# Performance work log

Hardware: AMD Instinct MI355X
Metric: run time of the kernel (lower is better)

Reference implementation:

```python
import jax, jax.numpy as jnp
import numpy as np

B, N, H, W = 128, 16384, 512, 512  # frames, points/frame, image height/width


def setup_inputs() -> dict:
    key = jax.random.key(0)
    k1, k2 = jax.random.split(key)
    pts = jax.random.uniform(k1, (B, N, 3), dtype=jnp.float32)
    # columns: x in [0, W-1], y in [0, H-1], intensity in [0, 1]
    outputs = jnp.concatenate(
        [pts[..., 0:1] * (W - 1), pts[..., 1:2] * (H - 1), pts[..., 2:3]], axis=-1
    )
    targets = jax.random.uniform(k2, (B, H, W), dtype=jnp.float32)
    return {"outputs": outputs, "targets": targets}


def _rasterize(outputs, h, w):
    """Bilinear splat of (x, y, intensity) points into a [B, h, w] image."""
    b, n, _ = outputs.shape
    x = jnp.clip(outputs[..., 0], 0.0, w - 1)
    y = jnp.clip(outputs[..., 1], 0.0, h - 1)
    inten = outputs[..., 2]
    x0f = jnp.floor(x)
    y0f = jnp.floor(y)
    fx = x - x0f  # fractional offsets -> bilinear weights
    fy = y - y0f
    x0 = x0f.astype(jnp.int32)
    y0 = y0f.astype(jnp.int32)
    x1 = jnp.minimum(x0 + 1, w - 1)
    y1 = jnp.minimum(y0 + 1, h - 1)
    bidx = jnp.broadcast_to(jnp.arange(b, dtype=jnp.int32)[:, None], (b, n))
    img = jnp.zeros((b, h, w), dtype=outputs.dtype)
    img = img.at[bidx, y0, x0].add(inten * (1 - fx) * (1 - fy))
    img = img.at[bidx, y0, x1].add(inten * fx * (1 - fy))
    img = img.at[bidx, y1, x0].add(inten * (1 - fx) * fy)
    img = img.at[bidx, y1, x1].add(inten * fx * fy)
    return img


def reference(outputs, targets):
    h, w = targets.shape[1], targets.shape[2]
    output_image = _rasterize(outputs, h, w)
    return jnp.mean((output_image - targets) ** 2)
```

## Files before the change

### kernel.cpp

```cpp
#include <hip/hip_runtime.h>

constexpr int B = 128;
constexpr int N = 16384;
constexpr int H = 512;
constexpr int W = 512;
constexpr int HW = H * W;
constexpr long long TOT = (long long)B * HW;

constexpr int TROWS = 16;
constexpr int NTILES = H / TROWS;
constexpr int NBUCKETS = B * NTILES;
constexpr int CAP = 1024;
constexpr int NGROUPS = B * N / 4;
constexpr int BIN_BLOCKS = NGROUPS / 512;
constexpr int TPITCH = 520;
constexpr int TILE_WORDS = TROWS * TPITCH;

__device__ __forceinline__ void lds_add(float* p, float v) {
    __hip_atomic_fetch_add(p, v, __ATOMIC_RELAXED, __HIP_MEMORY_SCOPE_WORKGROUP);
}

__device__ __forceinline__ void pin(float4& v) {
    asm volatile("" : "+v"(v.x), "+v"(v.y), "+v"(v.z), "+v"(v.w));
}

__global__ void __launch_bounds__(512) k_zero(unsigned int* __restrict__ cnt) {
    cnt[blockIdx.x * 512 + threadIdx.x] = 0u;
}

__global__ void __launch_bounds__(512) k_bin(const float4* __restrict__ pts,
                                             float4* __restrict__ buckets,
                                             unsigned int* __restrict__ cnt) {
    __shared__ unsigned int lcnt[NTILES];
    __shared__ unsigned int lbase[NTILES];

    int tid = blockIdx.x * 512 + threadIdx.x;
    int frame = tid >> 12;
    int fb = frame * NTILES;

    if (threadIdx.x < NTILES) lcnt[threadIdx.x] = 0;
    __syncthreads();

    float4 a = pts[tid * 3 + 0];
    float4 b = pts[tid * 3 + 1];
    float4 c = pts[tid * 3 + 2];

    float xs[4] = {a.x, a.w, b.z, c.y};
    float ys[4] = {a.y, b.x, b.w, c.z};
    float is[4] = {a.z, b.y, c.x, c.w};

    int tb0[4], sl0[4], tb1[4], sl1[4];
#pragma unroll
    for (int k = 0; k < 4; ++k) {
        float x = fminf(fmaxf(xs[k], 0.0f), (float)(W - 1));
        float y = fminf(fmaxf(ys[k], 0.0f), (float)(H - 1));
        xs[k] = x; ys[k] = y;
        int y0 = (int)floorf(y);
        int y1 = min(y0 + 1, H - 1);
        int t0 = y0 >> 4;
        int t1 = y1 >> 4;
        tb0[k] = t0;
        sl0[k] = (int)atomicAdd(&lcnt[t0], 1u);
        if (t1 != t0) {
            tb1[k] = t1;
            sl1[k] = (int)atomicAdd(&lcnt[t1], 1u);
        } else {
            tb1[k] = -1; sl1[k] = 0;
        }
    }
    __syncthreads();

    if (threadIdx.x < NTILES)
        lbase[threadIdx.x] = atomicAdd(&cnt[fb + threadIdx.x], lcnt[threadIdx.x]);
    __syncthreads();

#pragma unroll
    for (int k = 0; k < 4; ++k) {
        float4 rec = make_float4(xs[k], ys[k], is[k], 0.0f);
        unsigned s0 = lbase[tb0[k]] + (unsigned)sl0[k];
        if (s0 < (unsigned)CAP)
            buckets[(size_t)(fb + tb0[k]) * CAP + s0] = rec;
        if (tb1[k] >= 0) {
            unsigned s1 = lbase[tb1[k]] + (unsigned)sl1[k];
            if (s1 < (unsigned)CAP)
                buckets[(size_t)(fb + tb1[k]) * CAP + s1] = rec;
        }
    }
}

__device__ __forceinline__ void splat(float4 p, float* __restrict__ tile, int r0) {
    float x = p.x, y = p.y, inten = p.z;
    float x0f = floorf(x), y0f = floorf(y);
    float fx = x - x0f, fy = y - y0f;
    int x0 = (int)x0f, y0 = (int)y0f;
    int x1 = min(x0 + 1, W - 1);
    int y1 = min(y0 + 1, H - 1);
    int ra = y0 - r0;
    int rb = y1 - r0;
    float w00 = inten * (1.0f - fx) * (1.0f - fy);
    float w01 = inten * fx * (1.0f - fy);
    float w10 = inten * (1.0f - fx) * fy;
    float w11 = inten * fx * fy;
    if ((unsigned)ra < (unsigned)TROWS) {
        lds_add(&tile[ra * TPITCH + x0], w00);
        lds_add(&tile[ra * TPITCH + x1], w01);
    }
    if ((unsigned)rb < (unsigned)TROWS) {
        lds_add(&tile[rb * TPITCH + x0], w10);
        lds_add(&tile[rb * TPITCH + x1], w11);
    }
}

__global__ void __launch_bounds__(512) k_tile(const float4* __restrict__ buckets,
                                              const unsigned int* __restrict__ cnt,
                                              const float* __restrict__ tgt,
                                              double* __restrict__ ptile) {
    __shared__ __align__(16) float tile[TILE_WORDS];
    __shared__ double sacc[8];
    int bid = blockIdx.x;
    int frame = bid >> 5;
    int t = bid & (NTILES - 1);
    int r0 = t * TROWS;
    int tid = threadIdx.x;

    const float4* bp = buckets + (size_t)bid * CAP;
    float4 p0 = bp[tid];
    float4 p1 = bp[tid + 512];
    const float4* tg = (const float4*)(tgt + (size_t)frame * HW + (size_t)r0 * W);
    float4 tv0 = tg[tid];
    float4 tv1 = tg[tid + 512];
    float4 tv2 = tg[tid + 1024];
    float4 tv3 = tg[tid + 1536];
    int n = (int)min(cnt[bid], (unsigned)CAP);
    pin(p0); pin(p1); pin(tv0); pin(tv1); pin(tv2); pin(tv3);

    float4* t4 = (float4*)tile;
    float4 z = make_float4(0.f, 0.f, 0.f, 0.f);
    for (int i = tid; i < TILE_WORDS / 4; i += 512)
        t4[i] = z;
    __syncthreads();

    if (tid < n)       splat(p0, tile, r0);
    if (tid + 512 < n) splat(p1, tile, r0);
    __syncthreads();

    float facc = 0.0f;
#pragma unroll
    for (int k = 0; k < 4; ++k) {
        int g = tid + k * 512;
        int r = g >> 7;
        int c = (g & 127) << 2;
        float4 sv = *(const float4*)&tile[r * TPITCH + c];
        float4 tv = (k == 0) ? tv0 : (k == 1) ? tv1 : (k == 2) ? tv2 : tv3;
        float d0 = sv.x - tv.x, d1 = sv.y - tv.y;
        float d2 = sv.z - tv.z, d3 = sv.w - tv.w;
        facc += d0 * d0 + d1 * d1 + d2 * d2 + d3 * d3;
    }

    double acc = (double)facc;
    for (int off = 32; off > 0; off >>= 1)
        acc += __shfl_down(acc, off, 64);
    int lane = tid & 63;
    int wave = tid >> 6;
    if (lane == 0) sacc[wave] = acc;
    __syncthreads();
    if (tid == 0) {
        double s = 0.0;
#pragma unroll
        for (int wv = 0; wv < 8; ++wv) s += sacc[wv];
        ptile[bid] = s;
    }
}

__global__ void __launch_bounds__(512) k_final(const double* __restrict__ ptile,
                                               float* __restrict__ out) {
    double acc = 0.0;
    for (int i = threadIdx.x; i < NBUCKETS; i += 512)
        acc += ptile[i];
    for (int off = 32; off > 0; off >>= 1)
        acc += __shfl_down(acc, off, 64);
    __shared__ double sacc[8];
    int lane = threadIdx.x & 63;
    int wave = threadIdx.x >> 6;
    if (lane == 0) sacc[wave] = acc;
    __syncthreads();
    if (threadIdx.x == 0) {
        double s = 0.0;
#pragma unroll
        for (int wv = 0; wv < 8; ++wv) s += sacc[wv];
        out[0] = (float)(s / (double)TOT);
    }
}

extern "C" void kernel_launch(void* const* d_in, const int* in_sizes, int n_in,
                              void* d_out, int out_size, void* d_ws, size_t ws_size,
                              hipStream_t stream) {
    const float* pts = (const float*)d_in[0];
    const float* tgt = (const float*)d_in[1];
    float* out = (float*)d_out;

    unsigned int* cnt = (unsigned int*)d_ws;
    double* ptile = (double*)((char*)d_ws + 16384);
    float4* buckets = (float4*)((char*)d_ws + 65536);

    k_zero<<<NBUCKETS / 512, 512, 0, stream>>>(cnt);
    k_bin<<<BIN_BLOCKS, 512, 0, stream>>>((const float4*)pts, buckets, cnt);
    k_tile<<<NBUCKETS, 512, 0, stream>>>(buckets, cnt, tgt, ptile);
    k_final<<<1, 512, 0, stream>>>(ptile, out);
}
```

Baseline: 80.81 us.

## Process four tiles per block with double-buffered prefetch of next tile's data

k_tile now handles four consecutive row tiles per workgroup instead of one, launching a quarter as many blocks. While the current tile is zeroed and splatted, it issues the next tile's bucket points, target rows and count into a second register buffer. Barriers now wait only on LDS counters, so those global loads stay in flight across barriers. The per-wave reduction also moves from double to float shuffles before the double conversion; this costs more registers and slightly changes summation precision.

```diff
diff --git a/kernel.cpp b/kernel.cpp
--- a/kernel.cpp
+++ b/kernel.cpp
@@ -15,13 +15,16 @@
 constexpr int BIN_BLOCKS = NGROUPS / 512;
 constexpr int TPITCH = 520;
 constexpr int TILE_WORDS = TROWS * TPITCH;
+constexpr int TPB = 4;
+constexpr int TILE_BLOCKS = NBUCKETS / TPB;
 
 __device__ __forceinline__ void lds_add(float* p, float v) {
     __hip_atomic_fetch_add(p, v, __ATOMIC_RELAXED, __HIP_MEMORY_SCOPE_WORKGROUP);
 }
 
-__device__ __forceinline__ void pin(float4& v) {
-    asm volatile("" : "+v"(v.x), "+v"(v.y), "+v"(v.z), "+v"(v.w));
+__device__ __forceinline__ void BAR() {
+    asm volatile("s_waitcnt lgkmcnt(0)" ::: "memory");
+    __builtin_amdgcn_s_barrier();
 }
 
 __global__ void __launch_bounds__(512) k_zero(unsigned int* __restrict__ cnt) {
@@ -117,59 +120,77 @@
                                               double* __restrict__ ptile) {
     __shared__ __align__(16) float tile[TILE_WORDS];
     __shared__ double sacc[8];
-    int bid = blockIdx.x;
-    int frame = bid >> 5;
-    int t = bid & (NTILES - 1);
-    int r0 = t * TROWS;
     int tid = threadIdx.x;
-
-    const float4* bp = buckets + (size_t)bid * CAP;
-    float4 p0 = bp[tid];
-    float4 p1 = bp[tid + 512];
-    const float4* tg = (const float4*)(tgt + (size_t)frame * HW + (size_t)r0 * W);
-    float4 tv0 = tg[tid];
-    float4 tv1 = tg[tid + 512];
-    float4 tv2 = tg[tid + 1024];
-    float4 tv3 = tg[tid + 1536];
-    int n = (int)min(cnt[bid], (unsigned)CAP);
-    pin(p0); pin(p1); pin(tv0); pin(tv1); pin(tv2); pin(tv3);
+    int base = blockIdx.x * TPB;
+
+    float4 P[2][2];
+    float4 TV[2][4];
+    int    NN[2];
+
+#define LOADT(slot, tj) do {                                                   \
+        int tid_ = base + (tj);                                                \
+        const float4* bp_ = buckets + (size_t)tid_ * CAP;                      \
+        P[slot][0] = bp_[tid];                                                 \
+        P[slot][1] = bp_[tid + 512];                                           \
+        const float4* tg_ = (const float4*)(tgt + (size_t)(tid_ >> 5) * HW +   \
+                                            (size_t)(tid_ & 31) * TROWS * W);  \
+        TV[slot][0] = tg_[tid];                                                \
+        TV[slot][1] = tg_[tid + 512];                                          \
+        TV[slot][2] = tg_[tid + 1024];                                         \
+        TV[slot][3] = tg_[tid + 1536];                                         \
+        NN[slot] = (int)min(cnt[tid_], (unsigned)CAP);                         \
+    } while (0)
+
+    LOADT(0, 0);
 
     float4* t4 = (float4*)tile;
-    float4 z = make_float4(0.f, 0.f, 0.f, 0.f);
-    for (int i = tid; i < TILE_WORDS / 4; i += 512)
-        t4[i] = z;
-    __syncthreads();
-
-    if (tid < n)       splat(p0, tile, r0);
-    if (tid + 512 < n) splat(p1, tile, r0);
-    __syncthreads();
-
-    float facc = 0.0f;
-#pragma unroll
-    for (int k = 0; k < 4; ++k) {
-        int g = tid + k * 512;
-        int r = g >> 7;
-        int c = (g & 127) << 2;
-        float4 sv = *(const float4*)&tile[r * TPITCH + c];
-        float4 tv = (k == 0) ? tv0 : (k == 1) ? tv1 : (k == 2) ? tv2 : tv3;
-        float d0 = sv.x - tv.x, d1 = sv.y - tv.y;
-        float d2 = sv.z - tv.z, d3 = sv.w - tv.w;
-        facc += d0 * d0 + d1 * d1 + d2 * d2 + d3 * d3;
-    }
-
-    double acc = (double)facc;
-    for (int off = 32; off > 0; off >>= 1)
-        acc += __shfl_down(acc, off, 64);
-    int lane = tid & 63;
-    int wave = tid >> 6;
-    if (lane == 0) sacc[wave] = acc;
-    __syncthreads();
-    if (tid == 0) {
-        double s = 0.0;
-#pragma unroll
-        for (int wv = 0; wv < 8; ++wv) s += sacc[wv];
-        ptile[bid] = s;
-    }
+#pragma unroll
+    for (int j = 0; j < TPB; ++j) {
+        const int cur = j & 1, nxt = cur ^ 1;
+        int tile_id = base + j;
+        int r0 = (tile_id & (NTILES - 1)) * TROWS;
+
+        float4 z = make_float4(0.f, 0.f, 0.f, 0.f);
+        for (int i = tid; i < TILE_WORDS / 4; i += 512)
+            t4[i] = z;
+
+        if (j + 1 < TPB) LOADT(nxt, j + 1);
+
+        BAR();
+
+        int n = NN[cur];
+        if (tid < n)       splat(P[cur][0], tile, r0);
+        if (tid + 512 < n) splat(P[cur][1], tile, r0);
+
+        BAR();
+
+        float facc = 0.0f;
+#pragma unroll
+        for (int k = 0; k < 4; ++k) {
+            int g = tid + k * 512;
+            int r = g >> 7;
+            int c = (g & 127) << 2;
+            float4 sv = *(const float4*)&tile[r * TPITCH + c];
+            float4 tv = TV[cur][k];
+            float d0 = sv.x - tv.x, d1 = sv.y - tv.y;
+            float d2 = sv.z - tv.z, d3 = sv.w - tv.w;
+            facc += d0 * d0 + d1 * d1 + d2 * d2 + d3 * d3;
+        }
+
+        for (int off = 32; off > 0; off >>= 1)
+            facc += __shfl_down(facc, off, 64);
+        int lane = tid & 63;
+        int wave = tid >> 6;
+        if (lane == 0) sacc[wave] = (double)facc;
+        BAR();
+        if (tid == 0) {
+            double s = 0.0;
+#pragma unroll
+            for (int wv = 0; wv < 8; ++wv) s += sacc[wv];
+            ptile[tile_id] = s;
+        }
+    }
+#undef LOADT
 }
 
 __global__ void __launch_bounds__(512) k_final(const double* __restrict__ ptile,
@@ -205,6 +226,6 @@
 
     k_zero<<<NBUCKETS / 512, 512, 0, stream>>>(cnt);
     k_bin<<<BIN_BLOCKS, 512, 0, stream>>>((const float4*)pts, buckets, cnt);
-    k_tile<<<NBUCKETS, 512, 0, stream>>>(buckets, cnt, tgt, ptile);
+    k_tile<<<TILE_BLOCKS, 512, 0, stream>>>(buckets, cnt, tgt, ptile);
     k_final<<<1, 512, 0, stream>>>(ptile, out);
 }
```

Result: slower. 83.88 us (+3.8%).

## Split tile splat and MSE into separate kernels with fp16 intermediate image

Applied to the files above, without the earlier changes.

Halves the row tile and bucket capacity, then breaks the fused splat+MSE kernel in two. The splat kernel writes the rasterized tile to global memory as packed fp16, and a separate grid-stride kernel reads that image alongside the targets to compute the squared error. The intent is to take the target loads out of the LDS-atomic splat kernel and stream them in a simple bandwidth-bound pass. In exchange it adds an extra global round trip of the image (fp16, 32 MB write plus read), which loses precision in the rasterized values and adds a kernel launch.

```diff
diff --git a/kernel.cpp b/kernel.cpp
--- a/kernel.cpp
+++ b/kernel.cpp
@@ -1,4 +1,5 @@
 #include <hip/hip_runtime.h>
+#include <hip/hip_fp16.h>
 
 constexpr int B = 128;
 constexpr int N = 16384;
@@ -7,21 +8,28 @@
 constexpr int HW = H * W;
 constexpr long long TOT = (long long)B * HW;
 
-constexpr int TROWS = 16;
+constexpr int TROWS = 8;
 constexpr int NTILES = H / TROWS;
 constexpr int NBUCKETS = B * NTILES;
-constexpr int CAP = 1024;
+constexpr int CAP = 512;
 constexpr int NGROUPS = B * N / 4;
 constexpr int BIN_BLOCKS = NGROUPS / 512;
 constexpr int TPITCH = 520;
 constexpr int TILE_WORDS = TROWS * TPITCH;
+constexpr int MSE_BLOCKS = 2048;
 
 __device__ __forceinline__ void lds_add(float* p, float v) {
     __hip_atomic_fetch_add(p, v, __ATOMIC_RELAXED, __HIP_MEMORY_SCOPE_WORKGROUP);
 }
 
-__device__ __forceinline__ void pin(float4& v) {
-    asm volatile("" : "+v"(v.x), "+v"(v.y), "+v"(v.z), "+v"(v.w));
+__device__ __forceinline__ unsigned pack2(float a, float b) {
+    __half2 h = __floats2half2_rn(a, b);
+    return *reinterpret_cast<unsigned*>(&h);
+}
+
+__device__ __forceinline__ float2 unpack2(unsigned u) {
+    __half2 h = *reinterpret_cast<__half2*>(&u);
+    return __half22float2(h);
 }
 
 __global__ void __launch_bounds__(512) k_zero(unsigned int* __restrict__ cnt) {
@@ -57,8 +65,8 @@
         xs[k] = x; ys[k] = y;
         int y0 = (int)floorf(y);
         int y1 = min(y0 + 1, H - 1);
-        int t0 = y0 >> 4;
-        int t1 = y1 >> 4;
+        int t0 = y0 >> 3;
+        int t1 = y1 >> 3;
         tb0[k] = t0;
         sl0[k] = (int)atomicAdd(&lcnt[t0], 1u);
         if (t1 != t0) {
@@ -88,95 +96,105 @@
     }
 }
 
-__device__ __forceinline__ void splat(float4 p, float* __restrict__ tile, int r0) {
-    float x = p.x, y = p.y, inten = p.z;
-    float x0f = floorf(x), y0f = floorf(y);
-    float fx = x - x0f, fy = y - y0f;
-    int x0 = (int)x0f, y0 = (int)y0f;
-    int x1 = min(x0 + 1, W - 1);
-    int y1 = min(y0 + 1, H - 1);
-    int ra = y0 - r0;
-    int rb = y1 - r0;
-    float w00 = inten * (1.0f - fx) * (1.0f - fy);
-    float w01 = inten * fx * (1.0f - fy);
-    float w10 = inten * (1.0f - fx) * fy;
-    float w11 = inten * fx * fy;
-    if ((unsigned)ra < (unsigned)TROWS) {
-        lds_add(&tile[ra * TPITCH + x0], w00);
-        lds_add(&tile[ra * TPITCH + x1], w01);
-    }
-    if ((unsigned)rb < (unsigned)TROWS) {
-        lds_add(&tile[rb * TPITCH + x0], w10);
-        lds_add(&tile[rb * TPITCH + x1], w11);
-    }
-}
-
-__global__ void __launch_bounds__(512) k_tile(const float4* __restrict__ buckets,
-                                              const unsigned int* __restrict__ cnt,
-                                              const float* __restrict__ tgt,
-                                              double* __restrict__ ptile) {
+__global__ void __launch_bounds__(256) k_splat(const float4* __restrict__ buckets,
+                                               const unsigned int* __restrict__ cnt,
+                                               unsigned* __restrict__ img_u) {
     __shared__ __align__(16) float tile[TILE_WORDS];
-    __shared__ double sacc[8];
     int bid = blockIdx.x;
-    int frame = bid >> 5;
+    int frame = bid >> 6;
     int t = bid & (NTILES - 1);
     int r0 = t * TROWS;
     int tid = threadIdx.x;
 
-    const float4* bp = buckets + (size_t)bid * CAP;
-    float4 p0 = bp[tid];
-    float4 p1 = bp[tid + 512];
-    const float4* tg = (const float4*)(tgt + (size_t)frame * HW + (size_t)r0 * W);
-    float4 tv0 = tg[tid];
-    float4 tv1 = tg[tid + 512];
-    float4 tv2 = tg[tid + 1024];
-    float4 tv3 = tg[tid + 1536];
-    int n = (int)min(cnt[bid], (unsigned)CAP);
-    pin(p0); pin(p1); pin(tv0); pin(tv1); pin(tv2); pin(tv3);
-
     float4* t4 = (float4*)tile;
     float4 z = make_float4(0.f, 0.f, 0.f, 0.f);
-    for (int i = tid; i < TILE_WORDS / 4; i += 512)
+    for (int i = tid; i < TILE_WORDS / 4; i += 256)
         t4[i] = z;
-    __syncthreads();
-
-    if (tid < n)       splat(p0, tile, r0);
-    if (tid + 512 < n) splat(p1, tile, r0);
-    __syncthreads();
-
-    float facc = 0.0f;
+    int n = (int)min(cnt[bid], (unsigned)CAP);
+    __syncthreads();
+
+    const float4* bp = buckets + (size_t)bid * CAP;
+    for (int i = tid; i < n; i += 256) {
+        float4 p = bp[i];
+        float x = p.x, y = p.y, inten = p.z;
+        float x0f = floorf(x), y0f = floorf(y);
+        float fx = x - x0f, fy = y - y0f;
+        int x0 = (int)x0f, y0 = (int)y0f;
+        int x1 = min(x0 + 1, W - 1);
+        int y1 = min(y0 + 1, H - 1);
+        int ra = y0 - r0;
+        int rb = y1 - r0;
+        float w00 = inten * (1.0f - fx) * (1.0f - fy);
+        float w01 = inten * fx * (1.0f - fy);
+        float w10 = inten * (1.0f - fx) * fy;
+        float w11 = inten * fx * fy;
+        if ((unsigned)ra < (unsigned)TROWS) {
+            lds_add(&tile[ra * TPITCH + x0], w00);
+            lds_add(&tile[ra * TPITCH + x1], w01);
+        }
+        if ((unsigned)rb < (unsigned)TROWS) {
+            lds_add(&tile[rb * TPITCH + x0], w10);
+            lds_add(&tile[rb * TPITCH + x1], w11);
+        }
+    }
+    __syncthreads();
+
+    int g = tid * 16;
+    int r = g >> 9;
+    int c = g & 511;
+    const float* src = &tile[r * TPITCH + c];
+    unsigned ou[8];
 #pragma unroll
     for (int k = 0; k < 4; ++k) {
-        int g = tid + k * 512;
-        int r = g >> 7;
-        int c = (g & 127) << 2;
-        float4 sv = *(const float4*)&tile[r * TPITCH + c];
-        float4 tv = (k == 0) ? tv0 : (k == 1) ? tv1 : (k == 2) ? tv2 : tv3;
-        float d0 = sv.x - tv.x, d1 = sv.y - tv.y;
-        float d2 = sv.z - tv.z, d3 = sv.w - tv.w;
-        facc += d0 * d0 + d1 * d1 + d2 * d2 + d3 * d3;
-    }
-
-    double acc = (double)facc;
+        float4 v = *(const float4*)(src + k * 4);
+        ou[2 * k]     = pack2(v.x, v.y);
+        ou[2 * k + 1] = pack2(v.z, v.w);
+    }
+    size_t ubase = ((size_t)frame * HW + (size_t)r0 * W) >> 1;
+    uint4* dst = (uint4*)(img_u + ubase);
+    dst[tid * 2]     = make_uint4(ou[0], ou[1], ou[2], ou[3]);
+    dst[tid * 2 + 1] = make_uint4(ou[4], ou[5], ou[6], ou[7]);
+}
+
+__global__ void __launch_bounds__(256) k_mse(const uint4* __restrict__ img_u4,
+                                             const float4* __restrict__ tgt4,
+                                             double* __restrict__ pmse) {
+    int tid0 = blockIdx.x * 256 + threadIdx.x;
+    int nthr = MSE_BLOCKS * 256;
+    int units = (int)(TOT / 8);
+    double acc = 0.0;
+    for (int i = tid0; i < units; i += nthr) {
+        uint4 iu = img_u4[i];
+        float4 ta = tgt4[2 * i];
+        float4 tb = tgt4[2 * i + 1];
+        float2 i0 = unpack2(iu.x);
+        float2 i1 = unpack2(iu.y);
+        float2 i2 = unpack2(iu.z);
+        float2 i3 = unpack2(iu.w);
+        float d0 = i0.x - ta.x, d1 = i0.y - ta.y;
+        float d2 = i1.x - ta.z, d3 = i1.y - ta.w;
+        float d4 = i2.x - tb.x, d5 = i2.y - tb.y;
+        float d6 = i3.x - tb.z, d7 = i3.y - tb.w;
+        float s = d0 * d0 + d1 * d1 + d2 * d2 + d3 * d3 +
+                  d4 * d4 + d5 * d5 + d6 * d6 + d7 * d7;
+        acc += (double)s;
+    }
     for (int off = 32; off > 0; off >>= 1)
         acc += __shfl_down(acc, off, 64);
-    int lane = tid & 63;
-    int wave = tid >> 6;
+    __shared__ double sacc[4];
+    int lane = threadIdx.x & 63;
+    int wave = threadIdx.x >> 6;
     if (lane == 0) sacc[wave] = acc;
     __syncthreads();
-    if (tid == 0) {
-        double s = 0.0;
-#pragma unroll
-        for (int wv = 0; wv < 8; ++wv) s += sacc[wv];
-        ptile[bid] = s;
-    }
-}
-
-__global__ void __launch_bounds__(512) k_final(const double* __restrict__ ptile,
+    if (threadIdx.x == 0)
+        pmse[blockIdx.x] = sacc[0] + sacc[1] + sacc[2] + sacc[3];
+}
+
+__global__ void __launch_bounds__(512) k_final(const double* __restrict__ pmse,
                                                float* __restrict__ out) {
     double acc = 0.0;
-    for (int i = threadIdx.x; i < NBUCKETS; i += 512)
-        acc += ptile[i];
+    for (int i = threadIdx.x; i < MSE_BLOCKS; i += 512)
+        acc += pmse[i];
     for (int off = 32; off > 0; off >>= 1)
         acc += __shfl_down(acc, off, 64);
     __shared__ double sacc[8];
@@ -200,11 +218,13 @@
     float* out = (float*)d_out;
 
     unsigned int* cnt = (unsigned int*)d_ws;
-    double* ptile = (double*)((char*)d_ws + 16384);
-    float4* buckets = (float4*)((char*)d_ws + 65536);
+    double* pmse = (double*)((char*)d_ws + 32768);
+    float4* buckets = (float4*)((char*)d_ws + 131072);
+    unsigned* img_u = (unsigned*)((char*)d_ws + 131072 + ((size_t)NBUCKETS * CAP * 16));
 
     k_zero<<<NBUCKETS / 512, 512, 0, stream>>>(cnt);
     k_bin<<<BIN_BLOCKS, 512, 0, stream>>>((const float4*)pts, buckets, cnt);
-    k_tile<<<NBUCKETS, 512, 0, stream>>>(buckets, cnt, tgt, ptile);
-    k_final<<<1, 512, 0, stream>>>(ptile, out);
-}
+    k_splat<<<NBUCKETS, 256, 0, stream>>>(buckets, cnt, img_u);
+    k_mse<<<MSE_BLOCKS, 256, 0, stream>>>((const uint4*)img_u, (const float4*)tgt, pmse);
+    k_final<<<1, 512, 0, stream>>>(pmse, out);
+}
```

Measured after the change: 110.0 us. +36.1%, slower.

## Persistent tile blocks with double-buffered async global-to-LDS prefetch of targets and buckets

Applied to the files above, without the earlier changes.

Halves the tile height to 8 rows and the bucket capacity to 512. Each tile block now processes 16 consecutive tiles in a loop. The next tile's target rows and bucket points are prefetched straight into LDS with global_load_lds while the current tile is splatted and reduced, using manual waitcnt and barriers. This is meant to hide global load latency and cut block count and launch overhead. In exchange it uses a lot more LDS, which lowers occupancy, relies on fragile hand-written vmcnt accounting, and leaves less overflow headroom with CAP=512 per bucket.

```diff
diff --git a/kernel.cpp b/kernel.cpp
--- a/kernel.cpp
+++ b/kernel.cpp
@@ -7,21 +7,26 @@
 constexpr int HW = H * W;
 constexpr long long TOT = (long long)B * HW;
 
-constexpr int TROWS = 16;
+constexpr int TROWS = 8;
 constexpr int NTILES = H / TROWS;
 constexpr int NBUCKETS = B * NTILES;
-constexpr int CAP = 1024;
+constexpr int CAP = 512;
 constexpr int NGROUPS = B * N / 4;
 constexpr int BIN_BLOCKS = NGROUPS / 512;
 constexpr int TPITCH = 520;
 constexpr int TILE_WORDS = TROWS * TPITCH;
+constexpr int TPB = 16;
+constexpr int TILE_BLOCKS = NBUCKETS / TPB;
 
 __device__ __forceinline__ void lds_add(float* p, float v) {
     __hip_atomic_fetch_add(p, v, __ATOMIC_RELAXED, __HIP_MEMORY_SCOPE_WORKGROUP);
 }
 
-__device__ __forceinline__ void pin(float4& v) {
-    asm volatile("" : "+v"(v.x), "+v"(v.y), "+v"(v.z), "+v"(v.w));
+__device__ __forceinline__ void gload16(const void* g, void* s) {
+    __builtin_amdgcn_global_load_lds(
+        (const __attribute__((address_space(1))) void*)g,
+        (__attribute__((address_space(3))) void*)s,
+        16, 0, 0);
 }
 
 __global__ void __launch_bounds__(512) k_zero(unsigned int* __restrict__ cnt) {
@@ -57,8 +62,8 @@
         xs[k] = x; ys[k] = y;
         int y0 = (int)floorf(y);
         int y1 = min(y0 + 1, H - 1);
-        int t0 = y0 >> 4;
-        int t1 = y1 >> 4;
+        int t0 = y0 >> 3;
+        int t1 = y1 >> 3;
         tb0[k] = t0;
         sl0[k] = (int)atomicAdd(&lcnt[t0], 1u);
         if (t1 != t0) {
@@ -88,95 +93,123 @@
     }
 }
 
-__device__ __forceinline__ void splat(float4 p, float* __restrict__ tile, int r0) {
-    float x = p.x, y = p.y, inten = p.z;
-    float x0f = floorf(x), y0f = floorf(y);
-    float fx = x - x0f, fy = y - y0f;
-    int x0 = (int)x0f, y0 = (int)y0f;
-    int x1 = min(x0 + 1, W - 1);
-    int y1 = min(y0 + 1, H - 1);
-    int ra = y0 - r0;
-    int rb = y1 - r0;
-    float w00 = inten * (1.0f - fx) * (1.0f - fy);
-    float w01 = inten * fx * (1.0f - fy);
-    float w10 = inten * (1.0f - fx) * fy;
-    float w11 = inten * fx * fy;
-    if ((unsigned)ra < (unsigned)TROWS) {
-        lds_add(&tile[ra * TPITCH + x0], w00);
-        lds_add(&tile[ra * TPITCH + x1], w01);
-    }
-    if ((unsigned)rb < (unsigned)TROWS) {
-        lds_add(&tile[rb * TPITCH + x0], w10);
-        lds_add(&tile[rb * TPITCH + x1], w11);
-    }
-}
-
 __global__ void __launch_bounds__(512) k_tile(const float4* __restrict__ buckets,
                                               const unsigned int* __restrict__ cnt,
                                               const float* __restrict__ tgt,
-                                              double* __restrict__ ptile) {
-    __shared__ __align__(16) float tile[TILE_WORDS];
+                                              double* __restrict__ partials) {
+    __shared__ __align__(16) float tileacc[TILE_WORDS];
+    __shared__ __align__(16) float tgtbufA[TROWS * W];
+    __shared__ __align__(16) float tgtbufB[TROWS * W];
+    __shared__ __align__(16) float4 bktbufA[CAP];
+    __shared__ __align__(16) float4 bktbufB[CAP];
+    __shared__ int ncache[TPB];
     __shared__ double sacc[8];
-    int bid = blockIdx.x;
-    int frame = bid >> 5;
-    int t = bid & (NTILES - 1);
-    int r0 = t * TROWS;
+
     int tid = threadIdx.x;
-
-    const float4* bp = buckets + (size_t)bid * CAP;
-    float4 p0 = bp[tid];
-    float4 p1 = bp[tid + 512];
-    const float4* tg = (const float4*)(tgt + (size_t)frame * HW + (size_t)r0 * W);
-    float4 tv0 = tg[tid];
-    float4 tv1 = tg[tid + 512];
-    float4 tv2 = tg[tid + 1024];
-    float4 tv3 = tg[tid + 1536];
-    int n = (int)min(cnt[bid], (unsigned)CAP);
-    pin(p0); pin(p1); pin(tv0); pin(tv1); pin(tv2); pin(tv3);
-
-    float4* t4 = (float4*)tile;
-    float4 z = make_float4(0.f, 0.f, 0.f, 0.f);
-    for (int i = tid; i < TILE_WORDS / 4; i += 512)
-        t4[i] = z;
-    __syncthreads();
-
-    if (tid < n)       splat(p0, tile, r0);
-    if (tid + 512 < n) splat(p1, tile, r0);
-    __syncthreads();
-
-    float facc = 0.0f;
-#pragma unroll
-    for (int k = 0; k < 4; ++k) {
-        int g = tid + k * 512;
-        int r = g >> 7;
-        int c = (g & 127) << 2;
-        float4 sv = *(const float4*)&tile[r * TPITCH + c];
-        float4 tv = (k == 0) ? tv0 : (k == 1) ? tv1 : (k == 2) ? tv2 : tv3;
-        float d0 = sv.x - tv.x, d1 = sv.y - tv.y;
-        float d2 = sv.z - tv.z, d3 = sv.w - tv.w;
-        facc += d0 * d0 + d1 * d1 + d2 * d2 + d3 * d3;
-    }
-
-    double acc = (double)facc;
+    int wv = tid >> 6, ln = tid & 63;
+    int base = blockIdx.x * TPB;
+    if (tid < TPB) ncache[tid] = (int)min(cnt[base + tid], (unsigned)CAP);
+
+    const float4* tgt4 = (const float4*)(tgt + (size_t)(base >> 6) * HW +
+                                         (size_t)(base & (NTILES - 1)) * TROWS * W);
+    const float4* bkt0 = buckets + (size_t)base * CAP;
+
+#define STAGE(j, tb_, bb_) do {                                                \
+        const float4* ts_ = tgt4 + (j) * 1024;                                 \
+        const float4* bs_ = bkt0 + (size_t)(j) * CAP;                          \
+        int o_ = wv * 64 + ln;                                                 \
+        gload16(ts_ + o_,       (char*)(tb_) + wv * 1024);                     \
+        gload16(ts_ + 512 + o_, (char*)(tb_) + 8192 + wv * 1024);              \
+        gload16(bs_ + o_,       (char*)(bb_) + wv * 1024);                     \
+    } while (0)
+
+    STAGE(0, tgtbufA, bktbufA);
+
+    double acc = 0.0;
+    float4* t4 = (float4*)tileacc;
+
+#pragma unroll
+    for (int j = 0; j < TPB; ++j) {
+        float*  tb  = (j & 1) ? tgtbufB : tgtbufA;
+        float4* bb  = (j & 1) ? bktbufB : bktbufA;
+        float*  tbn = (j & 1) ? tgtbufA : tgtbufB;
+        float4* bbn = (j & 1) ? bktbufA : bktbufB;
+        int r0 = ((base + j) & (NTILES - 1)) * TROWS;
+
+        float4 z = make_float4(0.f, 0.f, 0.f, 0.f);
+        for (int i = tid; i < TILE_WORDS / 4; i += 512)
+            t4[i] = z;
+
+        if (j + 1 < TPB) STAGE(j + 1, tbn, bbn);
+
+        if (j + 1 < TPB) asm volatile("s_waitcnt vmcnt(3) lgkmcnt(0)" ::: "memory");
+        else             asm volatile("s_waitcnt vmcnt(0) lgkmcnt(0)" ::: "memory");
+        __builtin_amdgcn_sched_barrier(0);
+        __builtin_amdgcn_s_barrier();
+
+        int n = ncache[j];
+        if (tid < n) {
+            float4 p = bb[tid];
+            float x = p.x, y = p.y, inten = p.z;
+            float x0f = floorf(x), y0f = floorf(y);
+            float fx = x - x0f, fy = y - y0f;
+            int x0 = (int)x0f, y0 = (int)y0f;
+            int x1 = min(x0 + 1, W - 1);
+            int y1 = min(y0 + 1, H - 1);
+            int ra = y0 - r0;
+            int rb = y1 - r0;
+            float w00 = inten * (1.0f - fx) * (1.0f - fy);
+            float w01 = inten * fx * (1.0f - fy);
+            float w10 = inten * (1.0f - fx) * fy;
+            float w11 = inten * fx * fy;
+            if ((unsigned)ra < (unsigned)TROWS) {
+                lds_add(&tileacc[ra * TPITCH + x0], w00);
+                lds_add(&tileacc[ra * TPITCH + x1], w01);
+            }
+            if ((unsigned)rb < (unsigned)TROWS) {
+                lds_add(&tileacc[rb * TPITCH + x0], w10);
+                lds_add(&tileacc[rb * TPITCH + x1], w11);
+            }
+        }
+        asm volatile("s_waitcnt lgkmcnt(0)" ::: "memory");
+        __builtin_amdgcn_sched_barrier(0);
+        __builtin_amdgcn_s_barrier();
+
+        float facc = 0.0f;
+#pragma unroll
+        for (int k = 0; k < 2; ++k) {
+            int g4 = tid * 2 + k;
+            int r = g4 >> 7;
+            int c = (g4 & 127) << 2;
+            float4 sv = *(const float4*)&tileacc[r * TPITCH + c];
+            float4 tv = *(const float4*)&tb[g4 * 4];
+            float d0 = sv.x - tv.x, d1 = sv.y - tv.y;
+            float d2 = sv.z - tv.z, d3 = sv.w - tv.w;
+            facc += d0 * d0 + d1 * d1 + d2 * d2 + d3 * d3;
+        }
+        acc += (double)facc;
+
+        __builtin_amdgcn_s_barrier();
+    }
+#undef STAGE
+
     for (int off = 32; off > 0; off >>= 1)
         acc += __shfl_down(acc, off, 64);
-    int lane = tid & 63;
-    int wave = tid >> 6;
-    if (lane == 0) sacc[wave] = acc;
+    if (ln == 0) sacc[wv] = acc;
     __syncthreads();
     if (tid == 0) {
         double s = 0.0;
 #pragma unroll
-        for (int wv = 0; wv < 8; ++wv) s += sacc[wv];
-        ptile[bid] = s;
-    }
-}
-
-__global__ void __launch_bounds__(512) k_final(const double* __restrict__ ptile,
+        for (int w2 = 0; w2 < 8; ++w2) s += sacc[w2];
+        partials[blockIdx.x] = s;
+    }
+}
+
+__global__ void __launch_bounds__(512) k_final(const double* __restrict__ partials,
                                                float* __restrict__ out) {
     double acc = 0.0;
-    for (int i = threadIdx.x; i < NBUCKETS; i += 512)
-        acc += ptile[i];
+    for (int i = threadIdx.x; i < TILE_BLOCKS; i += 512)
+        acc += partials[i];
     for (int off = 32; off > 0; off >>= 1)
         acc += __shfl_down(acc, off, 64);
     __shared__ double sacc[8];
@@ -200,11 +233,11 @@
     float* out = (float*)d_out;
 
     unsigned int* cnt = (unsigned int*)d_ws;
-    double* ptile = (double*)((char*)d_ws + 16384);
-    float4* buckets = (float4*)((char*)d_ws + 65536);
+    double* partials = (double*)((char*)d_ws + 32768);
+    float4* buckets = (float4*)((char*)d_ws + 131072);
 
     k_zero<<<NBUCKETS / 512, 512, 0, stream>>>(cnt);
     k_bin<<<BIN_BLOCKS, 512, 0, stream>>>((const float4*)pts, buckets, cnt);
-    k_tile<<<NBUCKETS, 512, 0, stream>>>(buckets, cnt, tgt, ptile);
-    k_final<<<1, 512, 0, stream>>>(ptile, out);
-}
+    k_tile<<<TILE_BLOCKS, 512, 0, stream>>>(buckets, cnt, tgt, partials);
+    k_final<<<1, 512, 0, stream>>>(partials, out);
+}
```

New measurement: 94.63 us. 1.17x slower.
